# Performance work log

Measured on AMD Instinct MI355X. Metric: run time of the kernel, lower is better.

Reference implementation:

```python
import jax, jax.numpy as jnp
import numpy as np

HIDDEN = 1024
H2 = HIDDEN // 2
LAYERS = 2
NUM_CONDS = 4


def _lstm_dir(x, Wih, Whh, b, reverse):
    # x: (B, T, I); Wih: (4*H2, I); Whh: (4*H2, H2); b: (4*H2,)
    B = x.shape[0]
    h2 = Whh.shape[1]
    pre = jnp.einsum('bti,gi->btg', x, Wih) + b  # precompute input contribution
    pre = jnp.swapaxes(pre, 0, 1)  # (T, B, 4*H2)
    if reverse:
        pre = pre[::-1]

    def step(carry, g_in):
        h, c = carry
        g = g_in + h @ Whh.T
        i, f, gg, o = jnp.split(g, 4, axis=-1)
        c = jax.nn.sigmoid(f) * c + jax.nn.sigmoid(i) * jnp.tanh(gg)
        h = jax.nn.sigmoid(o) * jnp.tanh(c)
        return (h, c), h

    init = (jnp.zeros((B, h2), x.dtype), jnp.zeros((B, h2), x.dtype))
    _, hs = jax.lax.scan(step, init, pre)
    if reverse:
        hs = hs[::-1]
    return jnp.swapaxes(hs, 0, 1)  # (B, T, H2)


def _bilstm(x, Wih, Whh, b):
    # Wih: (L, 2, 4*H2, I) — all layers share input width since embed_dim == hidden_dim
    out = x
    for l in range(Wih.shape[0]):
        fwd = _lstm_dir(out, Wih[l, 0], Whh[l, 0], b[l, 0], False)
        bwd = _lstm_dir(out, Wih[l, 1], Whh[l, 1], b[l, 1], True)
        out = jnp.concatenate([fwd, bwd], axis=-1)
    return out


def setup_inputs() -> dict:
    key = jax.random.key(0)
    ks = jax.random.split(key, 24)
    s = 0.02
    G = 4 * H2
    inp = {
        'question_embedding': jax.random.normal(ks[0], (32, 128, 1024), jnp.float32),
        'packed_column_embedding': jax.random.normal(ks[1], (640, 8, 1024), jnp.float32),
        'gold_num': jax.random.randint(ks[2], (32,), 0, 5),
        'gold_cols': jax.random.randint(ks[3], (32, 4), 0, 20),
        'gold_ops': jax.random.randint(ks[4], (32, 4), 0, 4),
        'num_columns': 20,
        'q_Wih': jax.random.normal(ks[5], (LAYERS, 2, G, 1024), jnp.float32) * s,
        'q_Whh': jax.random.normal(ks[6], (LAYERS, 2, G, H2), jnp.float32) * s,
        'q_b': jax.random.normal(ks[7], (LAYERS, 2, G), jnp.float32) * s,
        'c_Wih': jax.random.normal(ks[8], (LAYERS, 2, G, 1024), jnp.float32) * s,
        'c_Whh': jax.random.normal(ks[9], (LAYERS, 2, G, H2), jnp.float32) * s,
        'c_b': jax.random.normal(ks[10], (LAYERS, 2, G), jnp.float32) * s,
        'col_attn_w': jax.random.normal(ks[11], (1, HIDDEN), jnp.float32) * s,
        'col_attn_b': jnp.zeros((1,), jnp.float32),
        'ob_attn_W': jax.random.normal(ks[12], (HIDDEN, HIDDEN), jnp.float32) * s,
        'ob_attn_b': jnp.zeros((HIDDEN,), jnp.float32),
        'ob_col_W': jax.random.normal(ks[13], (HIDDEN, HIDDEN), jnp.float32) * s,
        'ob_col_b': jnp.zeros((HIDDEN,), jnp.float32),
        'q_proj_W': jax.random.normal(ks[14], (HIDDEN, HIDDEN), jnp.float32) * s,
        'q_proj_b': jnp.zeros((HIDDEN,), jnp.float32),
        'out1_W': jax.random.normal(ks[15], (HIDDEN, 3 * HIDDEN), jnp.float32) * s,
        'out1_b': jnp.zeros((HIDDEN,), jnp.float32),
        'out2_W': jax.random.normal(ks[16], (2, HIDDEN), jnp.float32) * s,
        'out2_b': jnp.zeros((2,), jnp.float32),
    }
    return inp


def _forward(question_embedding, packed_column_embedding, gold_num, gold_cols,
             num_columns, q_Wih, q_Whh, q_b, c_Wih, c_Whh, c_b,
             col_attn_w, col_attn_b, ob_attn_W, ob_attn_b, ob_col_W, ob_col_b,
             q_proj_W, q_proj_b, out1_W, out1_b, out2_W, out2_b):
    dt = question_embedding.dtype
    bs, Tq, _ = question_embedding.shape
    # compute_mask: nonzero token positions
    q_mask = (jnp.abs(question_embedding).sum(-1) != 0).astype(dt)  # (B, Tq)
    c_mask = (jnp.abs(packed_column_embedding).sum(-1) != 0).astype(dt)  # (P, Tc)

    q_enc = _bilstm(question_embedding, q_Wih, q_Whh, q_b)  # (B, Tq, H)
    c_enc = _bilstm(packed_column_embedding, c_Wih, c_Whh, c_b)  # (P, Tc, H)

    # attention-pool each column name: make_weight = masked softmax over tokens
    logits = jnp.einsum('pth,oh->pt', c_enc, col_attn_w) + col_attn_b[0]
    logits = jnp.where(c_mask > 0, logits, -jnp.inf)
    w = jax.nn.softmax(logits, axis=-1)
    col_pooled = jnp.einsum('pt,pth->ph', w, c_enc)  # (P, H)
    column_hidden = col_pooled.reshape(bs, num_columns, HIDDEN)  # (B, NC, H)

    # get_observed_column_hidden (torch.no_grad): gather gold columns, zero-pad
    K = gold_cols.shape[1]
    gn = jnp.minimum(gold_num, K)
    cond_mask = (jnp.arange(K)[None, :] < gn[:, None]).astype(dt)  # (B, K)
    observed = jnp.take_along_axis(column_hidden, gold_cols[:, :, None], axis=1)  # (B, K, H)
    observed = observed * cond_mask[..., None]
    observed = jax.lax.stop_gradient(observed)
    cond_mask = jax.lax.stop_gradient(cond_mask)

    # mm_attention over question tokens
    att_key = observed @ ob_attn_W.T + ob_attn_b  # (B, K, H)
    scores = jnp.einsum('bkh,bqh->bkq', att_key, q_enc)
    scores = jnp.where(q_mask[:, None, :] > 0, scores, -jnp.inf)
    attn = jax.nn.softmax(scores, axis=-1)
    q_hidden = jnp.einsum('bkq,bqh->bkh', attn, q_enc)  # (B, K, H)

    vec = jnp.concatenate([observed @ ob_col_W.T + ob_col_b,
                           q_hidden @ q_proj_W.T + q_proj_b], axis=-1)  # (B, K, 2H)
    # broadcast concat: (B, K, Tq, 3H)
    x = jnp.concatenate([
        jnp.broadcast_to(q_enc[:, None], (bs, K, Tq, HIDDEN)),
        jnp.broadcast_to(vec[:, :, None], (bs, K, Tq, 2 * HIDDEN)),
    ], axis=-1)
    h1 = jnp.tanh(x @ out1_W.T + out1_b)
    pos = h1 @ out2_W.T + out2_b  # (B, K, Tq, 2)

    full_mask = cond_mask[:, :, None] * q_mask[:, None, :]  # (B, K, Tq)
    pos = jnp.where(full_mask[..., None] > 0, pos, -jnp.inf)
    return pos[..., 0], pos[..., 1]


def reference(question_embedding, packed_column_embedding, gold_num, gold_cols,
              gold_ops, num_columns, q_Wih, q_Whh, q_b, c_Wih, c_Whh, c_b,
              col_attn_w, col_attn_b, ob_attn_W, ob_attn_b, ob_col_W, ob_col_b,
              q_proj_W, q_proj_b, out1_W, out1_b, out2_W, out2_b):
    # gold_ops is accepted but unused by the original forward
    return _forward(question_embedding, packed_column_embedding, gold_num, gold_cols,
                    num_columns, q_Wih, q_Whh, q_b, c_Wih, c_Whh, c_b,
                    col_attn_w, col_attn_b, ob_attn_W, ob_attn_b, ob_col_W, ob_col_b,
                    q_proj_W, q_proj_b, out1_W, out1_b, out2_W, out2_b)
```

## Files before the change

kernel.cpp:

```cpp
#include <hip/hip_runtime.h>
#include <math.h>


using f32x4 = __attribute__((ext_vector_type(4))) float;
using s16x8 = __attribute__((ext_vector_type(8))) short;
typedef unsigned long long ulong_t;

#define ASYNC_COPY16(gsrc, ldst)                                               \
  __builtin_amdgcn_global_load_lds(                                            \
      (const __attribute__((address_space(1))) void*)(gsrc),                   \
      (__attribute__((address_space(3))) void*)(ldst), 16, 0, 0)

#define LSBM 0x0001000100010001ull

static __device__ __forceinline__ float sigm(float x) {
  return __builtin_amdgcn_rcpf(1.0f + __expf(-x));
}
static __device__ __forceinline__ float tanh_f(float x) {
  return 1.0f - 2.0f * __builtin_amdgcn_rcpf(__expf(2.0f * x) + 1.0f);
}

static __device__ __forceinline__ unsigned short f2b_one(float x) {
  unsigned int u = __float_as_uint(x);
  u = (u + 0x7FFFu + ((u >> 16) & 1u)) >> 16;
  return (unsigned short)u;
}

__global__ __launch_bounds__(256) void f2b_kernel(
    const float* __restrict__ in, unsigned short* __restrict__ out, int n4)
{
  const int i = blockIdx.x * 256 + threadIdx.x;
  if (i >= n4) return;
  const float4 v = ((const float4*)in)[i];
  ushort4 r;
  r.x = f2b_one(v.x); r.y = f2b_one(v.y);
  r.z = f2b_one(v.z); r.w = f2b_one(v.w);
  ((ushort4*)out)[i] = r;
}

__global__ __launch_bounds__(256) void mask_kernel(
    const float* __restrict__ qe, const float* __restrict__ pce,
    float* __restrict__ qmask, float* __restrict__ cmask)
{
  const int w = threadIdx.x >> 6;
  const int lane = threadIdx.x & 63;
  const int row = blockIdx.x * 4 + w;
  const float* src = (row < 4096) ? (qe + (size_t)row * 1024)
                                  : (pce + (size_t)(row - 4096) * 1024);
  float s = 0.f;
#pragma unroll
  for (int j = 0; j < 16; ++j) s += fabsf(src[lane + j * 64]);
#pragma unroll
  for (int off = 32; off > 0; off >>= 1) s += __shfl_down(s, off, 64);
  if (lane == 0) {
    const float m = (s != 0.f) ? 1.f : 0.f;
    if (row < 4096) qmask[row] = m;
    else cmask[row - 4096] = m;
  }
}

__global__ __launch_bounds__(256) void mfma_gemm_kernel(
    const unsigned short* __restrict__ X, const unsigned short* __restrict__ W,
    const float* __restrict__ bias, float* __restrict__ C,
    int K, int ldx, int ldw, int k0w, int ldc, int c0)
{
  __shared__ unsigned short As[128 * 32];
  __shared__ unsigned short Bs[128 * 32];
  const int tid = threadIdx.x;
  const int w = tid >> 6;
  const int l = tid & 63;
  const int m0 = blockIdx.y * 128;
  const int n0 = blockIdx.x * 128;
  const int wm = (w >> 1) * 64;
  const int wn = (w & 1) * 64;

  const unsigned short* xg =
      X + (size_t)(m0 + w * 32 + (l >> 2)) * ldx + (l & 3) * 8;
  const unsigned short* wgp =
      W + (size_t)(n0 + w * 32 + (l >> 2)) * ldw + k0w + (l & 3) * 8;
  unsigned short* asb = As + w * 1024;
  unsigned short* bsb = Bs + w * 1024;

  const int fr = l & 15;
  const int fq = l >> 4;
  const unsigned short* aRd = As + (wm + fr) * 32 + fq * 8;
  const unsigned short* bRd = Bs + (wn + fr) * 32 + fq * 8;

  f32x4 acc[4][4];
#pragma unroll
  for (int i = 0; i < 4; ++i)
#pragma unroll
    for (int j = 0; j < 4; ++j) acc[i][j] = (f32x4){0.f, 0.f, 0.f, 0.f};

  for (int k0 = 0; k0 < K; k0 += 32) {
    ASYNC_COPY16(xg + k0, asb);
    ASYNC_COPY16(xg + (size_t)16 * ldx + k0, asb + 512);
    ASYNC_COPY16(wgp + k0, bsb);
    ASYNC_COPY16(wgp + (size_t)16 * ldw + k0, bsb + 512);
    __syncthreads();
    s16x8 a[4], b[4];
#pragma unroll
    for (int i = 0; i < 4; ++i) a[i] = *(const s16x8*)(aRd + i * 512);
#pragma unroll
    for (int j = 0; j < 4; ++j) b[j] = *(const s16x8*)(bRd + j * 512);
#pragma unroll
    for (int i = 0; i < 4; ++i)
#pragma unroll
      for (int j = 0; j < 4; ++j)
        acc[i][j] = __builtin_amdgcn_mfma_f32_16x16x32_bf16(
            a[i], b[j], acc[i][j], 0, 0, 0);
    __syncthreads();
  }

#pragma unroll
  for (int j = 0; j < 4; ++j) {
    const int col = n0 + wn + j * 16 + fr;
    const float bj = bias ? bias[col] : 0.f;
#pragma unroll
    for (int i = 0; i < 4; ++i) {
      const int row = m0 + wm + i * 16 + fq * 4;
#pragma unroll
      for (int r = 0; r < 4; ++r)
        C[(size_t)(row + r) * ldc + c0 + col] = acc[i][j][r] + bj;
    }
  }
}

__global__ __launch_bounds__(256) void gemm_kernel(
    const float* __restrict__ X, const float* __restrict__ W,
    const float* __restrict__ bias, float* __restrict__ C,
    int M, int N, int K, int ldx, int ldw, int k0w, int ldc, int c0)
{
  __shared__ float Xs[16][68];
  __shared__ float Ws[16][68];
  const int tid = threadIdx.x;
  const int m0 = blockIdx.y * 64;
  const int n0 = blockIdx.x * 64;
  const int lrow = tid >> 2;
  const int lkk = (tid & 3) << 2;
  const float* Xp = X + (size_t)(m0 + lrow) * ldx + lkk;
  const float* Wp = W + (size_t)(n0 + lrow) * ldw + k0w + lkk;
  const int tm = (tid >> 4) << 2;
  const int tn = (tid & 15) << 2;
  float acc[4][4];
#pragma unroll
  for (int i = 0; i < 4; ++i)
#pragma unroll
    for (int j = 0; j < 4; ++j) acc[i][j] = 0.f;

  for (int k0 = 0; k0 < K; k0 += 16) {
    const float4 xv = *(const float4*)(Xp + k0);
    const float4 wv = *(const float4*)(Wp + k0);
    Xs[lkk + 0][lrow] = xv.x; Xs[lkk + 1][lrow] = xv.y;
    Xs[lkk + 2][lrow] = xv.z; Xs[lkk + 3][lrow] = xv.w;
    Ws[lkk + 0][lrow] = wv.x; Ws[lkk + 1][lrow] = wv.y;
    Ws[lkk + 2][lrow] = wv.z; Ws[lkk + 3][lrow] = wv.w;
    __syncthreads();
#pragma unroll
    for (int kk = 0; kk < 16; ++kk) {
      const float4 a4 = *(const float4*)&Xs[kk][tm];
      const float4 b4 = *(const float4*)&Ws[kk][tn];
      const float av[4] = {a4.x, a4.y, a4.z, a4.w};
      const float bv[4] = {b4.x, b4.y, b4.z, b4.w};
#pragma unroll
      for (int i = 0; i < 4; ++i)
#pragma unroll
        for (int j = 0; j < 4; ++j) acc[i][j] += av[i] * bv[j];
    }
    __syncthreads();
  }
  float bvv[4] = {0.f, 0.f, 0.f, 0.f};
  if (bias) {
#pragma unroll
    for (int j = 0; j < 4; ++j) bvv[j] = bias[n0 + tn + j];
  }
#pragma unroll
  for (int i = 0; i < 4; ++i)
#pragma unroll
    for (int j = 0; j < 4; ++j)
      C[(size_t)(m0 + tm + i) * ldc + c0 + n0 + tn + j] = acc[i][j] + bvv[j];
}

template <int NT>
__global__ __launch_bounds__(512) void lstm_seq_kernel(
    const float* __restrict__ pre,
    const unsigned short* __restrict__ whh,
    unsigned short* __restrict__ hbuf,
    float* __restrict__ out,
    int T, unsigned* __restrict__ bar, unsigned base)
{
  __shared__ float preS[NT][4][16][34];
  __shared__ float Tr[8][4][4][20];
  __shared__ unsigned short hR[NT * 16][528];
  const int tid = threadIdx.x;
  const int v = tid >> 6;
  const int l = tid & 63;
  const int d = blockIdx.x >> 4;
  const int w = blockIdx.x & 15;
  const int bg = blockIdx.y;
  const int fr = l & 15;
  const int fq = l >> 4;
  const int ubase = w * 32;
  const int unit = ubase + v * 4 + fq;
  const int nbase = bg * (NT * 16);
  const size_t SLOT = (size_t)640 * 512;
  unsigned* ctr = bar + (d * 8 + bg) * 16;
  unsigned short* sl = hbuf + (size_t)d * 3 * SLOT;

  s16x8 afr[16];
  {
    const unsigned short* arow = whh + (size_t)d * 2048 * 512 +
        ((size_t)(fr >> 2) * 512 + ubase + v * 4 + (fr & 3)) * 512 + fq * 8;
#pragma unroll
    for (int kk = 0; kk < 16; ++kk)
      afr[kk] = *(const s16x8*)(arow + kk * 32);
  }

  float creg[NT];
#pragma unroll
  for (int i = 0; i < NT; ++i) creg[i] = 0.f;

  const int sc = tid & 7;
  const int sn = (tid >> 3) & 15;
  const int sg = tid >> 7;

  for (int s = 0; s < 3; ++s) {
    ulong_t* cb = (ulong_t*)(sl + (size_t)s * SLOT + (size_t)nbase * 512 + ubase);
    for (int i = tid; i < NT * 16 * 8; i += 512)
      __hip_atomic_store(cb + (size_t)(i >> 3) * 128 + (i & 7), LSBM,
                         __ATOMIC_RELAXED, __HIP_MEMORY_SCOPE_AGENT);
  }
  {
    const int tt0 = d ? (T - 1) : 0;
#pragma unroll
    for (int nt = 0; nt < NT; ++nt) {
      const int n = nbase + nt * 16 + sn;
      const float4 pv = *(const float4*)(
          pre + ((size_t)n * T + tt0) * 4096 + d * 2048 + sg * 512 + ubase +
          sc * 4);
      *(float4*)&preS[nt][sg][sn][sc * 4] = pv;
    }
  }
  __syncthreads();
  if (tid == 0) {
    __hip_atomic_fetch_add(ctr, 1u, __ATOMIC_RELAXED,
                           __HIP_MEMORY_SCOPE_AGENT);
    const unsigned target = base + 16u;
    long spins = 0;
    while (__hip_atomic_load(ctr, __ATOMIC_RELAXED,
                             __HIP_MEMORY_SCOPE_AGENT) < target) {
      __builtin_amdgcn_s_sleep(1);
      if (++spins > 2000000L) break;
    }
  }
  __syncthreads();

  ulong_t u[4 * NT];
  for (int t = 0; t < T; ++t) {
    const int tt = d ? (T - 1 - t) : t;
    const unsigned wtag = (unsigned)((t / 3) & 1);
    unsigned short* wr = sl + (size_t)(t % 3) * SLOT;

    if (t > 0) {
      const unsigned rtag = (unsigned)(((t - 1) / 3) & 1);
      const ulong_t want = rtag ? LSBM : 0ull;
      const ulong_t* hq =
          (const ulong_t*)(sl + (size_t)((t + 2) % 3) * SLOT) +
          (size_t)nbase * 128;
      bool bad0 = false;
#pragma unroll
      for (int i = 0; i < 4 * NT; ++i) bad0 |= ((u[i] & LSBM) != want);
      if (bad0) {
        bool ok = false;
        int it = 0;
        while (!ok && it < 200000) {
#pragma unroll
          for (int i = 0; i < 2 * NT; ++i) {
            const int cid = i * 512 + tid;
            const ulong_t* p = hq + (size_t)(cid >> 6) * 128 + (cid & 63) * 2;
            u[2 * i] = __hip_atomic_load(p, __ATOMIC_RELAXED,
                                         __HIP_MEMORY_SCOPE_AGENT);
            u[2 * i + 1] = __hip_atomic_load(p + 1, __ATOMIC_RELAXED,
                                             __HIP_MEMORY_SCOPE_AGENT);
          }
          bool bad = false;
#pragma unroll
          for (int i = 0; i < 4 * NT; ++i) bad |= ((u[i] & LSBM) != want);
          ok = !bad;
          ++it;
          if (!ok && it > 8) __builtin_amdgcn_s_sleep(1);
        }
      }
#pragma unroll
      for (int i = 0; i < 2 * NT; ++i) {
        const int cid = i * 512 + tid;
        ulong_t* dst = (ulong_t*)&hR[cid >> 6][(cid & 63) * 8];
        dst[0] = u[2 * i];
        dst[1] = u[2 * i + 1];
      }
    }
    float4 pv[NT];
    if (t + 1 < T) {
      const int ttn = d ? (T - 2 - t) : (t + 1);
#pragma unroll
      for (int nt = 0; nt < NT; ++nt) {
        const int n = nbase + nt * 16 + sn;
        pv[nt] = *(const float4*)(
            pre + ((size_t)n * T + ttn) * 4096 + d * 2048 + sg * 512 + ubase +
            sc * 4);
      }
    }
    asm volatile("s_waitcnt lgkmcnt(0)" ::: "memory");
    __builtin_amdgcn_s_barrier();
    __builtin_amdgcn_sched_barrier(0);

#pragma unroll
    for (int nt = 0; nt < NT; ++nt) {
      f32x4 acc = (f32x4){0.f, 0.f, 0.f, 0.f};
      if (t > 0) {
        const unsigned short* bRd = &hR[nt * 16 + fr][fq * 8];
#pragma unroll
        for (int kk = 0; kk < 16; ++kk) {
          const s16x8 bv = *(const s16x8*)(bRd + kk * 32);
          acc = __builtin_amdgcn_mfma_f32_16x16x32_bf16(afr[kk], bv, acc,
                                                        0, 0, 0);
        }
      }
#pragma unroll
      for (int r = 0; r < 4; ++r) Tr[v][fq][r][fr] = acc[r];
      const int uu = v * 4 + fq;
      const float gi = Tr[v][0][fq][fr] + preS[nt][0][fr][uu];
      const float gf = Tr[v][1][fq][fr] + preS[nt][1][fr][uu];
      const float gg = Tr[v][2][fq][fr] + preS[nt][2][fr][uu];
      const float go = Tr[v][3][fq][fr] + preS[nt][3][fr][uu];
      const float cn = sigm(gf) * creg[nt] + sigm(gi) * tanh_f(gg);
      const float hn = sigm(go) * tanh_f(cn);
      creg[nt] = cn;
      const unsigned hv =
          (unsigned)((f2b_one(hn) & 0xFFFEu) | wtag);
      const unsigned pv16 = (unsigned)__shfl_xor((int)hv, 16, 64);
      const int n = nbase + nt * 16 + fr;
      if ((fq & 1) == 0) {
        const unsigned pk = hv | (pv16 << 16);
        __hip_atomic_store(
            (unsigned*)(wr + (size_t)n * 512) + (unit >> 1), pk,
            __ATOMIC_RELAXED, __HIP_MEMORY_SCOPE_AGENT);
      }
      out[((size_t)n * T + tt) * 1024 + d * 512 + unit] = hn;
    }
    asm volatile("s_waitcnt lgkmcnt(0)" ::: "memory");
    __builtin_amdgcn_s_barrier();
    __builtin_amdgcn_sched_barrier(0);

    if (t + 1 < T) {
#pragma unroll
      for (int nt = 0; nt < NT; ++nt)
        *(float4*)&preS[nt][sg][sn][sc * 4] = pv[nt];
      const ulong_t* hq =
          (const ulong_t*)(sl + (size_t)((t + 3) % 3) * SLOT) +
          (size_t)nbase * 128;
#pragma unroll
      for (int i = 0; i < 2 * NT; ++i) {
        const int cid = i * 512 + tid;
        const ulong_t* p = hq + (size_t)(cid >> 6) * 128 + (cid & 63) * 2;
        u[2 * i] = __hip_atomic_load(p, __ATOMIC_RELAXED,
                                     __HIP_MEMORY_SCOPE_AGENT);
        u[2 * i + 1] = __hip_atomic_load(p + 1, __ATOMIC_RELAXED,
                                         __HIP_MEMORY_SCOPE_AGENT);
      }
    }
  }
}

__global__ __launch_bounds__(256) void colpool_kernel(
    const float* __restrict__ cenc, const float* __restrict__ caw,
    const float* __restrict__ cab, const float* __restrict__ cmask,
    float* __restrict__ colh)
{
  __shared__ float part[8][33];
  __shared__ float wbuf[8];
  const int p = blockIdx.x;
  const int t = threadIdx.x >> 5;
  const int ln = threadIdx.x & 31;
  const float* row = cenc + ((size_t)p * 8 + t) * 1024;
  float s = 0.f;
  for (int j = ln; j < 1024; j += 32) s += row[j] * caw[j];
  part[t][ln] = s;
  __syncthreads();
  if (threadIdx.x < 8) {
    float lg = 0.f;
    for (int i = 0; i < 32; ++i) lg += part[threadIdx.x][i];
    lg += cab[0];
    wbuf[threadIdx.x] = (cmask[p * 8 + threadIdx.x] > 0.f) ? lg : -INFINITY;
  }
  __syncthreads();
  if (threadIdx.x == 0) {
    float mx = -INFINITY;
    for (int i = 0; i < 8; ++i) mx = fmaxf(mx, wbuf[i]);
    float e[8];
    float sum = 0.f;
    for (int i = 0; i < 8; ++i) { e[i] = __expf(wbuf[i] - mx); sum += e[i]; }
    for (int i = 0; i < 8; ++i) wbuf[i] = e[i] / sum;
  }
  __syncthreads();
  for (int h = threadIdx.x; h < 1024; h += 256) {
    float a = 0.f;
#pragma unroll
    for (int i = 0; i < 8; ++i) a += wbuf[i] * cenc[((size_t)p * 8 + i) * 1024 + h];
    colh[(size_t)p * 1024 + h] = a;
  }
}

__global__ __launch_bounds__(256) void gather_kernel(
    const float* __restrict__ colh, const int* __restrict__ gold_num,
    const int* __restrict__ gold_cols, const int* __restrict__ ncol,
    float* __restrict__ obs)
{
  const int idx = blockIdx.x * 256 + threadIdx.x;
  const int h = idx & 1023;
  const int k = (idx >> 10) & 3;
  const int b = idx >> 12;
  int gn = gold_num[b];
  if (gn > 4) gn = 4;
  const float m = (k < gn) ? 1.f : 0.f;
  const int col = gold_cols[b * 4 + k];
  const int NC = ncol[0];
  obs[idx] = m * colh[(size_t)(b * NC + col) * 1024 + h];
}

__global__ __launch_bounds__(128) void attn_kernel(
    const float* __restrict__ akey, const float* __restrict__ qenc,
    const float* __restrict__ qmask, float* __restrict__ qhid)
{
  __shared__ float ak[1024];
  __shared__ float red[128];
  __shared__ float at[128];
  const int bk = blockIdx.x;
  const int b = bk >> 2;
  const int tid = threadIdx.x;
  for (int i = tid; i < 1024; i += 128) ak[i] = akey[(size_t)bk * 1024 + i];
  __syncthreads();
  const float* qrow = qenc + ((size_t)b * 128 + tid) * 1024;
  float s = 0.f;
  for (int hh = 0; hh < 1024; hh += 4) {
    const float4 qv = *(const float4*)(qrow + hh);
    s += ak[hh] * qv.x + ak[hh + 1] * qv.y + ak[hh + 2] * qv.z + ak[hh + 3] * qv.w;
  }
  s = (qmask[b * 128 + tid] > 0.f) ? s : -INFINITY;
  at[tid] = s;
  red[tid] = s;
  __syncthreads();
  for (int off = 64; off > 0; off >>= 1) {
    if (tid < off) red[tid] = fmaxf(red[tid], red[tid + off]);
    __syncthreads();
  }
  const float mx = red[0];
  __syncthreads();
  const float e = __expf(at[tid] - mx);
  red[tid] = e;
  __syncthreads();
  for (int off = 64; off > 0; off >>= 1) {
    if (tid < off) red[tid] += red[tid + off];
    __syncthreads();
  }
  const float inv = 1.f / red[0];
  __syncthreads();
  at[tid] = e * inv;
  __syncthreads();
  for (int h = tid; h < 1024; h += 128) {
    float a = 0.f;
    for (int q = 0; q < 128; ++q)
      a += at[q] * qenc[((size_t)b * 128 + q) * 1024 + h];
    qhid[(size_t)bk * 1024 + h] = a;
  }
}

__global__ __launch_bounds__(64) void final_kernel(
    const float* __restrict__ A, const float* __restrict__ Bm,
    const float* __restrict__ w2, const float* __restrict__ b2,
    const int* __restrict__ gold_num, const float* __restrict__ qmask,
    float* __restrict__ out)
{
  const int bkq = blockIdx.x;
  const int q = bkq & 127;
  const int k = (bkq >> 7) & 3;
  const int b = bkq >> 9;
  int gn = gold_num[b];
  if (gn > 4) gn = 4;
  const bool act = (k < gn) && (qmask[b * 128 + q] > 0.f);
  const int lane = threadIdx.x;
  const int obase = (b * 4 + k) * 128 + q;
  if (!act) {
    if (lane == 0) {
      out[obase] = -1e30f;
      out[16384 + obase] = -1e30f;
    }
    return;
  }
  const float* Ar = A + ((size_t)b * 128 + q) * 1024;
  const float* Br = Bm + (size_t)(b * 4 + k) * 1024;
  float s0 = 0.f, s1 = 0.f;
  for (int o = lane; o < 1024; o += 64) {
    const float v = tanh_f(Ar[o] + Br[o]);
    s0 += v * w2[o];
    s1 += v * w2[1024 + o];
  }
#pragma unroll
  for (int off = 32; off > 0; off >>= 1) {
    s0 += __shfl_down(s0, off, 64);
    s1 += __shfl_down(s1, off, 64);
  }
  if (lane == 0) {
    out[obase] = s0 + b2[0];
    out[16384 + obase] = s1 + b2[1];
  }
}

extern "C" void kernel_launch(void* const* d_in, const int* in_sizes, int n_in,
                              void* d_out, int out_size, void* d_ws, size_t ws_size,
                              hipStream_t stream)
{
  const float* qe      = (const float*)d_in[0];
  const float* pce     = (const float*)d_in[1];
  const int* gold_num  = (const int*)d_in[2];
  const int* gold_cols = (const int*)d_in[3];
  const int* ncol      = (const int*)d_in[5];
  const float* q_Wih   = (const float*)d_in[6];
  const float* q_Whh   = (const float*)d_in[7];
  const float* q_b     = (const float*)d_in[8];
  const float* c_Wih   = (const float*)d_in[9];
  const float* c_Whh   = (const float*)d_in[10];
  const float* c_b     = (const float*)d_in[11];
  const float* caw     = (const float*)d_in[12];
  const float* cab     = (const float*)d_in[13];
  const float* obaW    = (const float*)d_in[14];
  const float* obab    = (const float*)d_in[15];
  const float* obcW    = (const float*)d_in[16];
  const float* obcb    = (const float*)d_in[17];
  const float* qpW     = (const float*)d_in[18];
  const float* qpb     = (const float*)d_in[19];
  const float* o1W     = (const float*)d_in[20];
  const float* o1b     = (const float*)d_in[21];
  const float* o2W     = (const float*)d_in[22];
  const float* o2b     = (const float*)d_in[23];
  float* outp = (float*)d_out;

  float* ws = (float*)d_ws;
  size_t off = 0;
  float* pre  = ws + off; off += 640UL * 8 * 4096;
  float* bufA = ws + off; off += 640UL * 8 * 1024;
  float* bufB = ws + off; off += 640UL * 8 * 1024;
  float* colh = ws + off; off += 640UL * 1024;
  float* qmask = ws + off; off += 4096;
  float* cmask = ws + off; off += 5120;
  float* obs  = ws + off; off += 131072;
  float* akey = ws + off; off += 131072;
  float* qhid = ws + off; off += 131072;
  float* vec  = ws + off; off += 262144;
  float* Bm   = ws + off; off += 131072;
  unsigned short* xb = (unsigned short*)(ws + off); off += 2621440;
  unsigned short* wb = (unsigned short*)(ws + off); off += 2097152;
  unsigned short* whhq = (unsigned short*)(ws + off); off += 2097152;
  unsigned short* whhc = (unsigned short*)(ws + off); off += 2097152;
  unsigned short* hbuf = (unsigned short*)(ws + off); off += 983040;
  unsigned* bar = (unsigned*)(ws + off); off += 256;
  float* Amat = pre;

  const dim3 blk(256);
  auto cvt = [&](const float* src, unsigned short* dst, int n) {
    hipLaunchKernelGGL(f2b_kernel, dim3((n / 4 + 255) / 256), blk, 0, stream,
                       src, dst, n / 4);
  };

  hipMemsetAsync(bar, 0, 1024, stream);

  hipLaunchKernelGGL(mask_kernel, dim3(2304), blk, 0, stream, qe, pce, qmask, cmask);

  cvt(q_Whh, whhq, 4194304);
  cvt(c_Whh, whhc, 4194304);

  for (int l = 0; l < 2; ++l) {
    const float* xin = (l == 0) ? pce : bufA;
    float* enc = (l == 0) ? bufA : bufB;
    cvt(xin, xb, 5242880);
    cvt(c_Wih + (size_t)l * 4194304, wb, 4194304);
    hipLaunchKernelGGL(mfma_gemm_kernel, dim3(4096 / 128, 5120 / 128), blk, 0,
                       stream, xb, wb, c_b + l * 4096, pre,
                       1024, 1024, 1024, 0, 4096, 0);
    hipLaunchKernelGGL((lstm_seq_kernel<5>), dim3(32, 8), dim3(512), 0, stream,
                       pre, whhc + (size_t)l * 2 * 2048 * 512, hbuf, enc,
                       8, bar, (unsigned)(l * 16));
  }
  hipLaunchKernelGGL(colpool_kernel, dim3(640), blk, 0, stream,
                     bufB, caw, cab, cmask, colh);
  hipLaunchKernelGGL(gather_kernel, dim3(512), blk, 0, stream,
                     colh, gold_num, gold_cols, ncol, obs);

  for (int l = 0; l < 2; ++l) {
    const float* xin = (l == 0) ? qe : bufA;
    float* enc = (l == 0) ? bufA : bufB;
    cvt(xin, xb, 4194304);
    cvt(q_Wih + (size_t)l * 4194304, wb, 4194304);
    hipLaunchKernelGGL(mfma_gemm_kernel, dim3(4096 / 128, 4096 / 128), blk, 0,
                       stream, xb, wb, q_b + l * 4096, pre,
                       1024, 1024, 1024, 0, 4096, 0);
    hipLaunchKernelGGL((lstm_seq_kernel<2>), dim3(32, 1), dim3(512), 0, stream,
                       pre, whhq + (size_t)l * 2 * 2048 * 512, hbuf, enc,
                       128, bar, (unsigned)(32 + l * 16));
  }
  const float* qenc = bufB;

  hipLaunchKernelGGL(gemm_kernel, dim3(16, 2), blk, 0, stream,
                     obs, obaW, obab, akey, 128, 1024, 1024, 1024, 1024, 0, 1024, 0);
  hipLaunchKernelGGL(attn_kernel, dim3(128), dim3(128), 0, stream,
                     akey, qenc, qmask, qhid);
  hipLaunchKernelGGL(gemm_kernel, dim3(16, 2), blk, 0, stream,
                     obs, obcW, obcb, vec, 128, 1024, 1024, 1024, 1024, 0, 2048, 0);
  hipLaunchKernelGGL(gemm_kernel, dim3(16, 2), blk, 0, stream,
                     qhid, qpW, qpb, vec, 128, 1024, 1024, 1024, 1024, 0, 2048, 1024);
  cvt(qenc, xb, 4194304);
  cvt(o1W, wb, 3145728);
  hipLaunchKernelGGL(mfma_gemm_kernel, dim3(1024 / 128, 4096 / 128), blk, 0,
                     stream, xb, wb, o1b, Amat, 1024, 1024, 3072, 0, 1024, 0);
  hipLaunchKernelGGL(gemm_kernel, dim3(16, 2), blk, 0, stream,
                     vec, o1W, nullptr, Bm, 128, 1024, 2048, 2048, 3072, 1024, 1024, 0);
  hipLaunchKernelGGL(final_kernel, dim3(16384), dim3(64), 0, stream,
                     Amat, Bm, o2W, o2b, gold_num, qmask, outp);
}
```

Measured before the change: 1.969 ms.

## Emit bf16 LSTM outputs directly and stage hidden-state publishes through LDS

The LSTM kernel gains an optional bf16 output, which feeds the next layer's GEMM and the final projection directly. This drops the separate fp32 store of layer-1 outputs and three float-to-bf16 conversion passes. The per-thread 32-bit atomic stores of the recurrent hidden state are replaced by staging into an LDS tile, then coalesced 64-bit atomic stores after the barrier. The global output writes are also moved after the barrier. The trade-off is extra LDS traffic and more work between the barrier and the next step's loads, which may lengthen the recurrent critical path.

Result: no change. 1.953 ms (-0.8%).

```diff
diff --git a/kernel.cpp b/kernel.cpp
--- a/kernel.cpp
+++ b/kernel.cpp
@@ -187,10 +187,12 @@
     const unsigned short* __restrict__ whh,
     unsigned short* __restrict__ hbuf,
     float* __restrict__ out,
+    unsigned short* __restrict__ outb,
     int T, unsigned* __restrict__ bar, unsigned base)
 {
   __shared__ float preS[NT][4][16][34];
   __shared__ float Tr[8][4][4][20];
+  __shared__ unsigned short hS[NT * 16][36];
   __shared__ unsigned short hR[NT * 16][528];
   const int tid = threadIdx.x;
   const int v = tid >> 6;
@@ -255,6 +257,7 @@
   }
   __syncthreads();
 
+  float hnreg[NT];
   ulong_t u[4 * NT];
   for (int t = 0; t < T; ++t) {
     const int tt = d ? (T - 1 - t) : t;
@@ -336,17 +339,9 @@
       const float cn = sigm(gf) * creg[nt] + sigm(gi) * tanh_f(gg);
       const float hn = sigm(go) * tanh_f(cn);
       creg[nt] = cn;
-      const unsigned hv =
-          (unsigned)((f2b_one(hn) & 0xFFFEu) | wtag);
-      const unsigned pv16 = (unsigned)__shfl_xor((int)hv, 16, 64);
-      const int n = nbase + nt * 16 + fr;
-      if ((fq & 1) == 0) {
-        const unsigned pk = hv | (pv16 << 16);
-        __hip_atomic_store(
-            (unsigned*)(wr + (size_t)n * 512) + (unit >> 1), pk,
-            __ATOMIC_RELAXED, __HIP_MEMORY_SCOPE_AGENT);
-      }
-      out[((size_t)n * T + tt) * 1024 + d * 512 + unit] = hn;
+      hnreg[nt] = hn;
+      hS[nt * 16 + fr][uu] =
+          (unsigned short)((f2b_one(hn) & 0xFFFEu) | wtag);
     }
     asm volatile("s_waitcnt lgkmcnt(0)" ::: "memory");
     __builtin_amdgcn_s_barrier();
@@ -356,9 +351,35 @@
 #pragma unroll
       for (int nt = 0; nt < NT; ++nt)
         *(float4*)&preS[nt][sg][sn][sc * 4] = pv[nt];
+    }
+    {
+      const int un = tid & 7;
+      const int nl = tid >> 3;
+      for (int p = nl; p < NT * 16; p += 64) {
+        const ulong_t val = *(const ulong_t*)&hS[p][un * 4];
+        __hip_atomic_store(
+            (ulong_t*)(wr + (size_t)(nbase + p) * 512 + ubase) + un, val,
+            __ATOMIC_RELAXED, __HIP_MEMORY_SCOPE_AGENT);
+      }
+    }
+    if (out) {
+#pragma unroll
+      for (int nt = 0; nt < NT; ++nt) {
+        const int n = nbase + nt * 16 + fr;
+        out[((size_t)n * T + tt) * 1024 + d * 512 + unit] = hnreg[nt];
+      }
+    }
+    if (outb) {
+#pragma unroll
+      for (int nt = 0; nt < NT; ++nt) {
+        const int n = nbase + nt * 16 + fr;
+        outb[((size_t)n * T + tt) * 1024 + d * 512 + unit] =
+            f2b_one(hnreg[nt]);
+      }
+    }
+    if (t + 1 < T) {
       const ulong_t* hq =
-          (const ulong_t*)(sl + (size_t)((t + 3) % 3) * SLOT) +
-          (size_t)nbase * 128;
+          (const ulong_t*)(sl + (size_t)(t % 3) * SLOT) + (size_t)nbase * 128;
 #pragma unroll
       for (int i = 0; i < 2 * NT; ++i) {
         const int cid = i * 512 + tid;
@@ -565,6 +586,7 @@
   unsigned short* hbuf = (unsigned short*)(ws + off); off += 983040;
   unsigned* bar = (unsigned*)(ws + off); off += 256;
   float* Amat = pre;
+  (void)bufA;
 
   const dim3 blk(256);
   auto cvt = [&](const float* src, unsigned short* dst, int n) {
@@ -579,35 +601,35 @@
   cvt(q_Whh, whhq, 4194304);
   cvt(c_Whh, whhc, 4194304);
 
-  for (int l = 0; l < 2; ++l) {
-    const float* xin = (l == 0) ? pce : bufA;
-    float* enc = (l == 0) ? bufA : bufB;
-    cvt(xin, xb, 5242880);
-    cvt(c_Wih + (size_t)l * 4194304, wb, 4194304);
-    hipLaunchKernelGGL(mfma_gemm_kernel, dim3(4096 / 128, 5120 / 128), blk, 0,
-                       stream, xb, wb, c_b + l * 4096, pre,
-                       1024, 1024, 1024, 0, 4096, 0);
-    hipLaunchKernelGGL((lstm_seq_kernel<5>), dim3(32, 8), dim3(512), 0, stream,
-                       pre, whhc + (size_t)l * 2 * 2048 * 512, hbuf, enc,
-                       8, bar, (unsigned)(l * 16));
-  }
+  cvt(pce, xb, 5242880);
+  cvt(c_Wih, wb, 4194304);
+  hipLaunchKernelGGL(mfma_gemm_kernel, dim3(4096 / 128, 5120 / 128), blk, 0,
+                     stream, xb, wb, c_b, pre, 1024, 1024, 1024, 0, 4096, 0);
+  hipLaunchKernelGGL((lstm_seq_kernel<5>), dim3(32, 8), dim3(512), 0, stream,
+                     pre, whhc, hbuf, (float*)nullptr, xb, 8, bar, 0u);
+  cvt(c_Wih + 4194304, wb, 4194304);
+  hipLaunchKernelGGL(mfma_gemm_kernel, dim3(4096 / 128, 5120 / 128), blk, 0,
+                     stream, xb, wb, c_b + 4096, pre, 1024, 1024, 1024, 0, 4096, 0);
+  hipLaunchKernelGGL((lstm_seq_kernel<5>), dim3(32, 8), dim3(512), 0, stream,
+                     pre, whhc + (size_t)2 * 2048 * 512, hbuf, bufB,
+                     (unsigned short*)nullptr, 8, bar, 16u);
   hipLaunchKernelGGL(colpool_kernel, dim3(640), blk, 0, stream,
                      bufB, caw, cab, cmask, colh);
   hipLaunchKernelGGL(gather_kernel, dim3(512), blk, 0, stream,
                      colh, gold_num, gold_cols, ncol, obs);
 
-  for (int l = 0; l < 2; ++l) {
-    const float* xin = (l == 0) ? qe : bufA;
-    float* enc = (l == 0) ? bufA : bufB;
-    cvt(xin, xb, 4194304);
-    cvt(q_Wih + (size_t)l * 4194304, wb, 4194304);
-    hipLaunchKernelGGL(mfma_gemm_kernel, dim3(4096 / 128, 4096 / 128), blk, 0,
-                       stream, xb, wb, q_b + l * 4096, pre,
-                       1024, 1024, 1024, 0, 4096, 0);
-    hipLaunchKernelGGL((lstm_seq_kernel<2>), dim3(32, 1), dim3(512), 0, stream,
-                       pre, whhq + (size_t)l * 2 * 2048 * 512, hbuf, enc,
-                       128, bar, (unsigned)(32 + l * 16));
-  }
+  cvt(qe, xb, 4194304);
+  cvt(q_Wih, wb, 4194304);
+  hipLaunchKernelGGL(mfma_gemm_kernel, dim3(4096 / 128, 4096 / 128), blk, 0,
+                     stream, xb, wb, q_b, pre, 1024, 1024, 1024, 0, 4096, 0);
+  hipLaunchKernelGGL((lstm_seq_kernel<2>), dim3(32, 1), dim3(512), 0, stream,
+                     pre, whhq, hbuf, (float*)nullptr, xb, 128, bar, 32u);
+  cvt(q_Wih + 4194304, wb, 4194304);
+  hipLaunchKernelGGL(mfma_gemm_kernel, dim3(4096 / 128, 4096 / 128), blk, 0,
+                     stream, xb, wb, q_b + 4096, pre, 1024, 1024, 1024, 0, 4096, 0);
+  hipLaunchKernelGGL((lstm_seq_kernel<2>), dim3(32, 1), dim3(512), 0, stream,
+                     pre, whhq + (size_t)2 * 2048 * 512, hbuf, bufB, xb,
+                     128, bar, 48u);
   const float* qenc = bufB;
 
   hipLaunchKernelGGL(gemm_kernel, dim3(16, 2), blk, 0, stream,
@@ -618,7 +640,6 @@
                      obs, obcW, obcb, vec, 128, 1024, 1024, 1024, 1024, 0, 2048, 0);
   hipLaunchKernelGGL(gemm_kernel, dim3(16, 2), blk, 0, stream,
                      qhid, qpW, qpb, vec, 128, 1024, 1024, 1024, 1024, 0, 2048, 1024);
-  cvt(qenc, xb, 4194304);
   cvt(o1W, wb, 3145728);
   hipLaunchKernelGGL(mfma_gemm_kernel, dim3(1024 / 128, 4096 / 128), blk, 0,
                      stream, xb, wb, o1b, Amat, 1024, 1024, 3072, 0, 1024, 0);
```
